# Optimization experiments

Hardware: AMD Instinct MI355X
Metric: run time of the kernel (lower is better)

The kernel has to match this reference:

```python
import jax, jax.numpy as jnp
import numpy as np

B, C, H, W = 8, 2048, 14, 14
NUM_CLASSES, WORD_DIM, INTER_DIM = 80, 300, 1024


def setup_inputs() -> dict:
    key = jax.random.key(0)
    ks = jax.random.split(key, 8)
    s = 0.02
    return {
        "image_features": jax.random.normal(ks[0], (B, C, H, W), jnp.float32),
        "word_features": jax.random.normal(ks[1], (NUM_CLASSES, WORD_DIM), jnp.float32),
        "W1": jax.random.normal(ks[2], (INTER_DIM, C), jnp.float32) * s,
        "W2": jax.random.normal(ks[3], (INTER_DIM, WORD_DIM), jnp.float32) * s,
        "W3": jax.random.normal(ks[4], (INTER_DIM, INTER_DIM), jnp.float32) * s,
        "b3": jax.random.normal(ks[5], (INTER_DIM,), jnp.float32) * s,
        "Wa": jax.random.normal(ks[6], (1, INTER_DIM), jnp.float32) * s,
        "ba": jax.random.normal(ks[7], (1,), jnp.float32) * s,
        "num_classes": NUM_CLASSES,
    }


def reference(image_features, word_features, W1, W2, W3, b3, Wa, ba, num_classes):
    b, c, h, w = image_features.shape
    # [s, b, c] with s = h*w (spatial locations)
    img = image_features.reshape(b, c, h * w).transpose(2, 0, 1)
    f_wh = img @ W1.T                      # [s, b, D]
    f_wd = word_features @ W2.T            # [n, D]
    # additive-attention score MLP; broadcast to [s, b, n, D]
    lb = jnp.tanh(f_wh[:, :, None, :] * f_wd[None, None, :, :]) @ W3.T + b3
    coef = (lb @ Wa.T + ba)[..., 0]        # [s, b, n]
    coef = jax.nn.softmax(coef, axis=0)    # softmax over spatial locations
    # weighted sum over spatial dim -> [b, n, c]
    return jnp.einsum('sbc,sbn->bnc', img, coef)
```

## Files before the change

kernel.cpp:

```cpp
#include <hip/hip_runtime.h>
#include <math.h>

#define SB 196
#define SP 224
#define NB 8
#define NC 2048
#define ND 1024
#define NN 80
#define NW 300
#define CH 8
#define DCH (ND / CH)
#define NJ (NB * SB)
#define NJP 1600
#define PITCH 40

typedef __bf16 v8bf __attribute__((ext_vector_type(8)));
typedef __bf16 v4bf __attribute__((ext_vector_type(4)));
typedef float  f32x4 __attribute__((ext_vector_type(4)));

__global__ __launch_bounds__(256) void kcast_x(const float* __restrict__ X,
                                               const float* __restrict__ W1,
                                               const float* __restrict__ W3,
                                               const float* __restrict__ Wa,
                                               __bf16* __restrict__ Xt,
                                               __bf16* __restrict__ Xhi,
                                               __bf16* __restrict__ Xlo,
                                               __bf16* __restrict__ W1b,
                                               float* __restrict__ vpart) {
    const int t = threadIdx.x;
    if (blockIdx.z == 9) {
        if (blockIdx.x < 16) {
            const int e0 = blockIdx.x * 64;
            const int d  = blockIdx.y * 256 + t;
            float p = 0.f;
            #pragma unroll 8
            for (int e = e0; e < e0 + 64; ++e)
                p += Wa[e] * W3[(size_t)e * ND + d];
            vpart[blockIdx.x * ND + d] = p;
        } else if (blockIdx.x == 16) {
            const int tid = blockIdx.y * 256 + t;
            uint4 z = make_uint4(0u, 0u, 0u, 0u);
            uint4* p = (uint4*)(Xt + (size_t)NJ * NC);
            #pragma unroll
            for (int r = 0; r < 8; ++r) p[tid + r * 1024] = z;
        }
        return;
    }
    if (blockIdx.z == 8) {
        unsigned int slice_tid = (blockIdx.x * 4 + blockIdx.y) * 256 + t;
        #pragma unroll 4
        for (int r = 0; r < 16; ++r) {
            size_t i = ((size_t)slice_tid + (size_t)r * 32768) * 4;
            float4 f = *(const float4*)(W1 + i);
            v4bf o;
            o[0] = (__bf16)f.x; o[1] = (__bf16)f.y;
            o[2] = (__bf16)f.z; o[3] = (__bf16)f.w;
            *(v4bf*)(W1b + i) = o;
        }
        return;
    }
    __shared__ float tile[64][65];
    const int b  = blockIdx.z;
    const int c0 = blockIdx.x * 64;
    const int s0 = blockIdx.y * 64;
    const float* Xb = X + (size_t)b * NC * SB;
    {
        int ss = t & 63, cbase = t >> 6;
        #pragma unroll
        for (int r = 0; r < 16; ++r) {
            int cc = cbase + 4 * r;
            float val = (s0 + ss < SB) ? Xb[(size_t)(c0 + cc) * SB + s0 + ss] : 0.f;
            tile[cc][ss] = val;
        }
    }
    __syncthreads();
    {
        int cc = t & 63, sbase = t >> 6;
        #pragma unroll
        for (int r = 0; r < 16; ++r) {
            int ss = sbase + 4 * r;
            if (s0 + ss < SB)
                Xt[((size_t)b * SB + s0 + ss) * NC + c0 + cc] = (__bf16)tile[cc][ss];
        }
    }
    {
        int ss = t & 63, cbase = t >> 6;
        int sg = s0 + ss;
        #pragma unroll
        for (int r = 0; r < 16; ++r) {
            int cc = cbase + 4 * r;
            if (sg < SP) {
                float val = (sg < SB) ? tile[cc][ss] : 0.f;
                __bf16 h = (__bf16)val;
                __bf16 l = (__bf16)(val - (float)h);
                size_t base = ((size_t)b * NC + c0 + cc) * SP + sg;
                Xhi[base] = h;
                Xlo[base] = l;
            }
        }
    }
}

__global__ __launch_bounds__(256) void k1_mfma(const __bf16* __restrict__ Xt,
                                               const __bf16* __restrict__ W1b,
                                               float* __restrict__ F,
                                               const float* __restrict__ word,
                                               const float* __restrict__ W2,
                                               const float* __restrict__ vpart,
                                               float2* __restrict__ wpack) {
    const int t = threadIdx.x;
    if (blockIdx.y >= 25) {
        __shared__ __align__(16) float lword[NW];
        const int e = (blockIdx.y - 25) * 16 + blockIdx.x;
        const int n = e >> 2;
        const int d = (e & 3) * 256 + t;
        for (int i = t; i < NW; i += 256) lword[i] = word[(size_t)n * NW + i];
        __syncthreads();
        const float4* wr = (const float4*)(W2 + (size_t)d * NW);
        const float4* l4 = (const float4*)lword;
        float acc = 0.f;
        #pragma unroll 5
        for (int i = 0; i < NW / 4; ++i) {
            float4 a = wr[i], b = l4[i];
            acc += a.x * b.x + a.y * b.y + a.z * b.z + a.w * b.w;
        }
        float vv = 0.f;
        #pragma unroll
        for (int p = 0; p < 16; ++p) vv += vpart[p * ND + d];
        float2 o;
        o.x = 2.8853900817779268f * acc;
        o.y = -2.f * vv;
        wpack[(size_t)n * ND + d] = o;
        return;
    }
    __shared__ __align__(16) __bf16 lA[64 * PITCH];
    __shared__ __align__(16) __bf16 lB[64 * PITCH];
    const int d0   = blockIdx.x * 64;
    const int j0   = blockIdx.y * 64;
    const int lane = t & 63;
    const int wave = t >> 6;
    const int doff = (wave & 1) * 32;
    const int joff = (wave >> 1) * 32;
    const int quad = lane >> 4;
    const int l16  = lane & 15;

    f32x4 acc[2][2] = {};

    const int rr = t >> 2;
    const int cc = (t & 3) * 8;
    const __bf16* Ag = W1b + (size_t)(d0 + rr) * NC + cc;
    const __bf16* Bg = Xt + (size_t)(j0 + rr) * NC + cc;
    __bf16* lAw = lA + rr * PITCH + cc;
    __bf16* lBw = lB + rr * PITCH + cc;

    const __bf16* rA0 = lA + (doff + l16) * PITCH + quad * 8;
    const __bf16* rA1 = rA0 + 16 * PITCH;
    const __bf16* rB0 = lB + (joff + l16) * PITCH + quad * 8;
    const __bf16* rB1 = rB0 + 16 * PITCH;

    for (int k0 = 0; k0 < NC; k0 += 32) {
        uint4 a  = *(const uint4*)(Ag + k0);
        uint4 bv = *(const uint4*)(Bg + k0);
        __syncthreads();
        *(uint4*)lAw = a;
        *(uint4*)lBw = bv;
        __syncthreads();
        v8bf a0 = *(const v8bf*)rA0;
        v8bf a1 = *(const v8bf*)rA1;
        v8bf b0 = *(const v8bf*)rB0;
        v8bf b1 = *(const v8bf*)rB1;
        acc[0][0] = __builtin_amdgcn_mfma_f32_16x16x32_bf16(a0, b0, acc[0][0], 0, 0, 0);
        acc[0][1] = __builtin_amdgcn_mfma_f32_16x16x32_bf16(a0, b1, acc[0][1], 0, 0, 0);
        acc[1][0] = __builtin_amdgcn_mfma_f32_16x16x32_bf16(a1, b0, acc[1][0], 0, 0, 0);
        acc[1][1] = __builtin_amdgcn_mfma_f32_16x16x32_bf16(a1, b1, acc[1][1], 0, 0, 0);
    }
    #pragma unroll
    for (int i = 0; i < 2; ++i) {
        #pragma unroll
        for (int jj = 0; jj < 2; ++jj) {
            int j = j0 + joff + jj * 16 + l16;
            if (j < NJ) {
                int b = j / SB;
                int s = j - b * SB;
                float* Fp = F + ((size_t)b * ND + d0 + doff + i * 16 + quad * 4) * SB + s;
                #pragma unroll
                for (int r = 0; r < 4; ++r)
                    Fp[(size_t)r * SB] = acc[i][jj][r];
            }
        }
    }
}

__global__ __launch_bounds__(256) void k2a(const float* __restrict__ F,
                                           const float2* __restrict__ wpack,
                                           float* __restrict__ part) {
    const int n0  = blockIdx.x * 4;
    const int ch  = blockIdx.z;
    const int idx = blockIdx.y * 256 + threadIdx.x;
    const bool valid = idx < (NB * SB);
    const int iv = valid ? idx : 0;
    const int b  = iv / SB;
    const int s  = iv - b * SB;
    const float*  Fp  = F + ((size_t)b * ND + ch * DCH) * SB + s;
    const float4* wp0 = (const float4*)(wpack + (size_t)(n0 + 0) * ND + ch * DCH);
    const float4* wp1 = (const float4*)(wpack + (size_t)(n0 + 1) * ND + ch * DCH);
    const float4* wp2 = (const float4*)(wpack + (size_t)(n0 + 2) * ND + ch * DCH);
    const float4* wp3 = (const float4*)(wpack + (size_t)(n0 + 3) * ND + ch * DCH);
    float a0 = 0.f, a1 = 0.f, a2 = 0.f, a3 = 0.f;
    #pragma unroll 4
    for (int d2 = 0; d2 < DCH / 2; ++d2) {
        float f0 = Fp[(size_t)(2 * d2)     * SB];
        float f1 = Fp[(size_t)(2 * d2 + 1) * SB];
        float4 w0 = wp0[d2];
        float4 w1 = wp1[d2];
        float4 w2 = wp2[d2];
        float4 w3 = wp3[d2];
        float e00 = __builtin_amdgcn_exp2f(f0 * w0.x);
        float e01 = __builtin_amdgcn_exp2f(f1 * w0.z);
        float e10 = __builtin_amdgcn_exp2f(f0 * w1.x);
        float e11 = __builtin_amdgcn_exp2f(f1 * w1.z);
        float e20 = __builtin_amdgcn_exp2f(f0 * w2.x);
        float e21 = __builtin_amdgcn_exp2f(f1 * w2.z);
        float e30 = __builtin_amdgcn_exp2f(f0 * w3.x);
        float e31 = __builtin_amdgcn_exp2f(f1 * w3.z);
        a0 = fmaf(w0.y, __builtin_amdgcn_rcpf(1.f + e00), a0);
        a0 = fmaf(w0.w, __builtin_amdgcn_rcpf(1.f + e01), a0);
        a1 = fmaf(w1.y, __builtin_amdgcn_rcpf(1.f + e10), a1);
        a1 = fmaf(w1.w, __builtin_amdgcn_rcpf(1.f + e11), a1);
        a2 = fmaf(w2.y, __builtin_amdgcn_rcpf(1.f + e20), a2);
        a2 = fmaf(w2.w, __builtin_amdgcn_rcpf(1.f + e21), a2);
        a3 = fmaf(w3.y, __builtin_amdgcn_rcpf(1.f + e30), a3);
        a3 = fmaf(w3.w, __builtin_amdgcn_rcpf(1.f + e31), a3);
    }
    if (valid) {
        size_t base = ((size_t)ch * NB + b) * NN;
        part[(base + n0 + 0) * 256 + s] = a0;
        part[(base + n0 + 1) * 256 + s] = a1;
        part[(base + n0 + 2) * 256 + s] = a2;
        part[(base + n0 + 3) * 256 + s] = a3;
    }
}

__global__ __launch_bounds__(256) void k2b(const float* __restrict__ part,
                                           __bf16* __restrict__ coefh,
                                           __bf16* __restrict__ coefl) {
    __shared__ float red[256];
    const int n = blockIdx.x;
    const int b = blockIdx.y;
    const int t = threadIdx.x;
    float acc = 0.f;
    #pragma unroll
    for (int ch = 0; ch < CH; ++ch)
        acc += part[(((size_t)ch * NB + b) * NN + n) * 256 + t];

    red[t] = (t < SB) ? acc : -1e30f;
    __syncthreads();
    #pragma unroll
    for (int off = 128; off > 0; off >>= 1) {
        if (t < off) red[t] = fmaxf(red[t], red[t + off]);
        __syncthreads();
    }
    float m = red[0];
    __syncthreads();
    float p = (t < SB) ? __expf(acc - m) : 0.f;
    red[t] = p;
    __syncthreads();
    #pragma unroll
    for (int off = 128; off > 0; off >>= 1) {
        if (t < off) red[t] += red[t + off];
        __syncthreads();
    }
    float inv = 1.f / red[0];
    if (t < SP) {
        float val = (t < SB) ? p * inv : 0.f;
        __bf16 h = (__bf16)val;
        __bf16 l = (__bf16)(val - (float)h);
        size_t base = ((size_t)b * NN + n) * SP + t;
        coefh[base] = h;
        coefl[base] = l;
    }
}

__global__ __launch_bounds__(256) void k3_mfma(const __bf16* __restrict__ Xhi,
                                               const __bf16* __restrict__ Xlo,
                                               const __bf16* __restrict__ coefh,
                                               const __bf16* __restrict__ coefl,
                                               float* __restrict__ out) {
    const int t     = threadIdx.x;
    const int wave  = t >> 6;
    const int lane  = t & 63;
    const int quad  = lane >> 4;
    const int l16   = lane & 15;
    const int b     = blockIdx.y;
    const int cbase = blockIdx.x * 64 + wave * 16;

    const __bf16* Bh = Xhi + ((size_t)b * NC + cbase + l16) * SP + quad * 8;
    const __bf16* Bl = Xlo + ((size_t)b * NC + cbase + l16) * SP + quad * 8;
    const __bf16* Ah = coefh + ((size_t)b * NN + l16) * SP + quad * 8;
    const __bf16* Al = coefl + ((size_t)b * NN + l16) * SP + quad * 8;

    f32x4 acc[5] = {};

    #pragma unroll
    for (int k0 = 0; k0 < SP; k0 += 32) {
        v8bf bh = *(const v8bf*)(Bh + k0);
        v8bf bl = *(const v8bf*)(Bl + k0);
        #pragma unroll
        for (int mt = 0; mt < 5; ++mt) {
            v8bf ah = *(const v8bf*)(Ah + (size_t)mt * 16 * SP + k0);
            v8bf al = *(const v8bf*)(Al + (size_t)mt * 16 * SP + k0);
            acc[mt] = __builtin_amdgcn_mfma_f32_16x16x32_bf16(ah, bh, acc[mt], 0, 0, 0);
            acc[mt] = __builtin_amdgcn_mfma_f32_16x16x32_bf16(al, bh, acc[mt], 0, 0, 0);
            acc[mt] = __builtin_amdgcn_mfma_f32_16x16x32_bf16(ah, bl, acc[mt], 0, 0, 0);
        }
    }
    #pragma unroll
    for (int mt = 0; mt < 5; ++mt) {
        #pragma unroll
        for (int r = 0; r < 4; ++r) {
            int n = mt * 16 + quad * 4 + r;
            out[((size_t)b * NN + n) * NC + cbase + l16] = acc[mt][r];
        }
    }
}

extern "C" void kernel_launch(void* const* d_in, const int* in_sizes, int n_in,
                              void* d_out, int out_size, void* d_ws, size_t ws_size,
                              hipStream_t stream) {
    const float* X    = (const float*)d_in[0];
    const float* word = (const float*)d_in[1];
    const float* W1   = (const float*)d_in[2];
    const float* W2   = (const float*)d_in[3];
    const float* W3   = (const float*)d_in[4];
    const float* Wa   = (const float*)d_in[6];
    float* out = (float*)d_out;

    char* ws = (char*)d_ws;
    float*  vpart = (float*)ws;
    float2* wpack = (float2*)(vpart + 16 * ND);
    float*  part  = (float*)(wpack + (size_t)NN * ND);
    __bf16* coefh = (__bf16*)(part + (size_t)CH * NB * NN * 256);
    __bf16* coefl = coefh + (size_t)NB * NN * SP;
    __bf16* W1b   = coefl + (size_t)NB * NN * SP;
    __bf16* Xt    = W1b + (size_t)ND * NC;
    float*  F     = (float*)(Xt + (size_t)NJP * NC);
    __bf16* Xhi   = (__bf16*)(F + (size_t)NB * ND * SB);
    __bf16* Xlo   = Xhi + (size_t)NB * NC * SP;

    kcast_x<<<dim3(32, 4, 10),   256, 0, stream>>>(X, W1, W3, Wa, Xt, Xhi, Xlo, W1b, vpart);
    k1_mfma<<<dim3(16, 45),      256, 0, stream>>>(Xt, W1b, F, word, W2, vpart, wpack);
    k2a    <<<dim3(NN / 4, 7, CH), 256, 0, stream>>>(F, wpack, part);
    k2b    <<<dim3(NN, NB),      256, 0, stream>>>(part, coefh, coefl);
    k3_mfma<<<dim3(NC / 64, NB), 256, 0, stream>>>(Xhi, Xlo, coefh, coefl, out);
}
```

Before: 169.1 us.

## Fuse attention score reduction with softmax into a single kernel

Merges the chunked score kernel and the softmax kernel into one kernel per (class, batch) that loops over the full hidden dimension, staging the packed weights in shared memory. This removes the partial-sum buffer, its global round trip, and one launch. In exchange each block re-reads the full feature slice for its batch with no reuse across classes, and there are fewer, longer blocks.

```diff
diff --git a/kernel.cpp b/kernel.cpp
--- a/kernel.cpp
+++ b/kernel.cpp
@@ -8,8 +8,6 @@
 #define ND 1024
 #define NN 80
 #define NW 300
-#define CH 8
-#define DCH (ND / CH)
 #define NJ (NB * SB)
 #define NJP 1600
 #define PITCH 40
@@ -191,68 +189,41 @@
     }
 }
 
-__global__ __launch_bounds__(256) void k2a(const float* __restrict__ F,
+__global__ __launch_bounds__(256) void k2f(const float* __restrict__ F,
                                            const float2* __restrict__ wpack,
-                                           float* __restrict__ part) {
-    const int n0  = blockIdx.x * 4;
-    const int ch  = blockIdx.z;
-    const int idx = blockIdx.y * 256 + threadIdx.x;
-    const bool valid = idx < (NB * SB);
-    const int iv = valid ? idx : 0;
-    const int b  = iv / SB;
-    const int s  = iv - b * SB;
-    const float*  Fp  = F + ((size_t)b * ND + ch * DCH) * SB + s;
-    const float4* wp0 = (const float4*)(wpack + (size_t)(n0 + 0) * ND + ch * DCH);
-    const float4* wp1 = (const float4*)(wpack + (size_t)(n0 + 1) * ND + ch * DCH);
-    const float4* wp2 = (const float4*)(wpack + (size_t)(n0 + 2) * ND + ch * DCH);
-    const float4* wp3 = (const float4*)(wpack + (size_t)(n0 + 3) * ND + ch * DCH);
-    float a0 = 0.f, a1 = 0.f, a2 = 0.f, a3 = 0.f;
-    #pragma unroll 4
-    for (int d2 = 0; d2 < DCH / 2; ++d2) {
-        float f0 = Fp[(size_t)(2 * d2)     * SB];
-        float f1 = Fp[(size_t)(2 * d2 + 1) * SB];
-        float4 w0 = wp0[d2];
-        float4 w1 = wp1[d2];
-        float4 w2 = wp2[d2];
-        float4 w3 = wp3[d2];
-        float e00 = __builtin_amdgcn_exp2f(f0 * w0.x);
-        float e01 = __builtin_amdgcn_exp2f(f1 * w0.z);
-        float e10 = __builtin_amdgcn_exp2f(f0 * w1.x);
-        float e11 = __builtin_amdgcn_exp2f(f1 * w1.z);
-        float e20 = __builtin_amdgcn_exp2f(f0 * w2.x);
-        float e21 = __builtin_amdgcn_exp2f(f1 * w2.z);
-        float e30 = __builtin_amdgcn_exp2f(f0 * w3.x);
-        float e31 = __builtin_amdgcn_exp2f(f1 * w3.z);
-        a0 = fmaf(w0.y, __builtin_amdgcn_rcpf(1.f + e00), a0);
-        a0 = fmaf(w0.w, __builtin_amdgcn_rcpf(1.f + e01), a0);
-        a1 = fmaf(w1.y, __builtin_amdgcn_rcpf(1.f + e10), a1);
-        a1 = fmaf(w1.w, __builtin_amdgcn_rcpf(1.f + e11), a1);
-        a2 = fmaf(w2.y, __builtin_amdgcn_rcpf(1.f + e20), a2);
-        a2 = fmaf(w2.w, __builtin_amdgcn_rcpf(1.f + e21), a2);
-        a3 = fmaf(w3.y, __builtin_amdgcn_rcpf(1.f + e30), a3);
-        a3 = fmaf(w3.w, __builtin_amdgcn_rcpf(1.f + e31), a3);
-    }
-    if (valid) {
-        size_t base = ((size_t)ch * NB + b) * NN;
-        part[(base + n0 + 0) * 256 + s] = a0;
-        part[(base + n0 + 1) * 256 + s] = a1;
-        part[(base + n0 + 2) * 256 + s] = a2;
-        part[(base + n0 + 3) * 256 + s] = a3;
-    }
-}
-
-__global__ __launch_bounds__(256) void k2b(const float* __restrict__ part,
                                            __bf16* __restrict__ coefh,
                                            __bf16* __restrict__ coefl) {
+    __shared__ __align__(16) float2 lw[ND];
     __shared__ float red[256];
     const int n = blockIdx.x;
     const int b = blockIdx.y;
     const int t = threadIdx.x;
-    float acc = 0.f;
-    #pragma unroll
-    for (int ch = 0; ch < CH; ++ch)
-        acc += part[(((size_t)ch * NB + b) * NN + n) * 256 + t];
-
+    {
+        const float4* src = (const float4*)(wpack + (size_t)n * ND);
+        float4* dst = (float4*)lw;
+        dst[t]       = src[t];
+        dst[t + 256] = src[t + 256];
+    }
+    __syncthreads();
+    const int s = (t < SB) ? t : 0;
+    const float* Fp = F + (size_t)b * ND * SB + s;
+    float a0 = 0.f, a1 = 0.f, a2 = 0.f, a3 = 0.f;
+    #pragma unroll 2
+    for (int d = 0; d < ND; d += 4) {
+        float f0 = Fp[(size_t)(d + 0) * SB];
+        float f1 = Fp[(size_t)(d + 1) * SB];
+        float f2 = Fp[(size_t)(d + 2) * SB];
+        float f3 = Fp[(size_t)(d + 3) * SB];
+        float2 w0 = lw[d + 0];
+        float2 w1 = lw[d + 1];
+        float2 w2 = lw[d + 2];
+        float2 w3 = lw[d + 3];
+        a0 = fmaf(w0.y, __builtin_amdgcn_rcpf(1.f + __builtin_amdgcn_exp2f(f0 * w0.x)), a0);
+        a1 = fmaf(w1.y, __builtin_amdgcn_rcpf(1.f + __builtin_amdgcn_exp2f(f1 * w1.x)), a1);
+        a2 = fmaf(w2.y, __builtin_amdgcn_rcpf(1.f + __builtin_amdgcn_exp2f(f2 * w2.x)), a2);
+        a3 = fmaf(w3.y, __builtin_amdgcn_rcpf(1.f + __builtin_amdgcn_exp2f(f3 * w3.x)), a3);
+    }
+    float acc = (a0 + a1) + (a2 + a3);
     red[t] = (t < SB) ? acc : -1e30f;
     __syncthreads();
     #pragma unroll
@@ -338,8 +309,7 @@
     char* ws = (char*)d_ws;
     float*  vpart = (float*)ws;
     float2* wpack = (float2*)(vpart + 16 * ND);
-    float*  part  = (float*)(wpack + (size_t)NN * ND);
-    __bf16* coefh = (__bf16*)(part + (size_t)CH * NB * NN * 256);
+    __bf16* coefh = (__bf16*)(wpack + (size_t)NN * ND);
     __bf16* coefl = coefh + (size_t)NB * NN * SP;
     __bf16* W1b   = coefl + (size_t)NB * NN * SP;
     __bf16* Xt    = W1b + (size_t)ND * NC;
@@ -349,7 +319,6 @@
 
     kcast_x<<<dim3(32, 4, 10),   256, 0, stream>>>(X, W1, W3, Wa, Xt, Xhi, Xlo, W1b, vpart);
     k1_mfma<<<dim3(16, 45),      256, 0, stream>>>(Xt, W1b, F, word, W2, vpart, wpack);
-    k2a    <<<dim3(NN / 4, 7, CH), 256, 0, stream>>>(F, wpack, part);
-    k2b    <<<dim3(NN, NB),      256, 0, stream>>>(part, coefh, coefl);
+    k2f    <<<dim3(NN, NB),      256, 0, stream>>>(F, wpack, coefh, coefl);
     k3_mfma<<<dim3(NC / 64, NB), 256, 0, stream>>>(Xhi, Xlo, coefh, coefl, out);
 }
```

Result: slower. 189.6 us (+12.1%).
